# Performance work log

Measured on AMD Instinct MI355X. Metric: run time of the kernel, lower is better.

## Reference

```python
import jax, jax.numpy as jnp
import numpy as np

D_MODEL = 1024
B, S = 4, 2048


def setup_inputs() -> dict:
    key = jax.random.key(0)
    kx, km, kq, kk, kv, ko = jax.random.split(key, 6)
    x = jax.random.normal(kx, (B, S, D_MODEL), dtype=jnp.float32)
    mask = jax.random.randint(km, (B, S, S), 0, 2).astype(jnp.bool_)
    # flax Dense default kernel init: lecun_normal-ish; plain scaled normal is fine for a reference
    init_scale = 1.0 / np.sqrt(D_MODEL)
    Wq = jax.random.normal(kq, (D_MODEL, D_MODEL), dtype=jnp.float32) * init_scale
    Wk = jax.random.normal(kk, (D_MODEL, D_MODEL), dtype=jnp.float32) * init_scale
    Wv = jax.random.normal(kv, (D_MODEL, D_MODEL), dtype=jnp.float32) * init_scale
    Wo = jax.random.normal(ko, (D_MODEL, D_MODEL), dtype=jnp.float32) * init_scale
    return {"x": x, "mask": mask, "Wq": Wq, "Wk": Wk, "Wv": Wv, "Wo": Wo}


def reference(x, mask, Wq, Wk, Wv, Wo):
    # QKV projections (use_bias=False)
    q = jnp.einsum('bsd,de->bse', x, Wq)
    k = jnp.einsum('bsd,de->bse', x, Wk)
    v = jnp.einsum('bsd,de->bse', x, Wv)
    scale = jnp.sqrt(jnp.asarray(q.shape[-1], x.dtype)).astype(x.dtype)
    # [B, S, S] attention scores
    attn_scores = jnp.einsum('bqd,bkd->bqk', q, k) / scale
    attn_scores = jnp.where(mask, attn_scores, jnp.asarray(-1e10, x.dtype))
    attn_weights = jax.nn.softmax(attn_scores, axis=-1)
    attn_output = jnp.einsum('bqk,bkd->bqd', attn_weights, v)
    return jnp.einsum('bsd,de->bse', attn_output, Wo)
```

## Files before the change

kernel.cpp:

```cpp
#include <hip/hip_runtime.h>


#define DM 1024
#define SQ 2048
#define NB 4
typedef unsigned short U16;
typedef short bhalf8 __attribute__((ext_vector_type(8)));
typedef float f32x4 __attribute__((ext_vector_type(4)));

__device__ inline U16 f2bf(float f) {
  unsigned int u = __float_as_uint(f);
  u += 0x7FFFu + ((u >> 16) & 1u);
  return (U16)(u >> 16);
}
__device__ inline float2 bfp2(unsigned int u) {
  float2 r;
  r.x = __uint_as_float(u << 16);
  r.y = __uint_as_float(u & 0xffff0000u);
  return r;
}
__device__ inline unsigned int packbf(float a, float b) {
  return (unsigned int)f2bf(a) | ((unsigned int)f2bf(b) << 16);
}

__global__ __launch_bounds__(256) void conv_f32_bf16(
    const float* __restrict__ src, U16* __restrict__ dst) {
  int i = (blockIdx.x * 256 + threadIdx.x) * 8;
  float4 a = *(const float4*)(src + i);
  float4 b = *(const float4*)(src + i + 4);
  uint4 w;
  w.x = packbf(a.x, a.y); w.y = packbf(a.z, a.w);
  w.z = packbf(b.x, b.y); w.w = packbf(b.z, b.w);
  *(uint4*)(dst + i) = w;
}

__device__ inline void ldcvt16(const float* p, U16* d) {
#pragma unroll
  for (int i = 0; i < 4; ++i) {
    float4 f = *(const float4*)(p + i * 4);
    d[i * 4 + 0] = f2bf(f.x); d[i * 4 + 1] = f2bf(f.y);
    d[i * 4 + 2] = f2bf(f.z); d[i * 4 + 3] = f2bf(f.w);
  }
}
__device__ inline void ldcvt16(const U16* p, U16* d) {
  uint4 a = *(const uint4*)p;
  uint4 b = *(const uint4*)(p + 8);
  *(uint4*)d = a;
  *(uint4*)(d + 8) = b;
}
template <typename TIN>
__global__ __launch_bounds__(256) void transp_to_bf16(
    const TIN* __restrict__ src, U16* __restrict__ dst, int R, int C) {
  __shared__ U16 tile[64][72];
  const int z = blockIdx.z;
  src += (size_t)z * R * C;
  dst += (size_t)z * R * C;
  const int r0 = blockIdx.y * 64, c0 = blockIdx.x * 64;
  const int t = threadIdx.x;
  const int tr = t >> 2, tc = (t & 3) * 16;
  ldcvt16(src + (size_t)(r0 + tr) * C + c0 + tc, &tile[tr][tc]);
  __syncthreads();
  U16 vals[16];
#pragma unroll
  for (int m = 0; m < 16; ++m) vals[m] = tile[tc + m][tr];
  U16* op = dst + (size_t)(c0 + tr) * R + r0 + tc;
  *(uint4*)op = *(uint4*)&vals[0];
  *(uint4*)(op + 8) = *(uint4*)&vals[8];
}

template <int EP>
__global__ __launch_bounds__(256) void gemm_mfma(
    const U16* __restrict__ A, const U16* __restrict__ B, void* __restrict__ Cv,
    int M, int N, int K, long long sA, long long sB, long long sC,
    const int* __restrict__ mask, const float* __restrict__ rowsum, float scale) {
  __shared__ U16 As[128 * 72];
  __shared__ U16 Bs[128 * 72];
  const int t = threadIdx.x;
  const int lane = t & 63, wave = t >> 6;
  const int wm = wave >> 1, wn = wave & 1;
  const int q = lane >> 4, ln = lane & 15;
  const int z = blockIdx.z;
  const int m0 = blockIdx.y * 128, n0 = blockIdx.x * 128;
  A += (size_t)z * sA;
  B += (size_t)z * sB;

  f32x4 acc[4][4] = {};

  const int srow = t >> 3;
  const int scol = (t & 7) * 8;

  for (int k0 = 0; k0 < K; k0 += 64) {
    const U16* ga = A + (size_t)(m0 + srow) * K + k0 + scol;
    const U16* gb = B + (size_t)(n0 + srow) * K + k0 + scol;
#pragma unroll
    for (int it = 0; it < 4; ++it) {
      uint4 va = *(const uint4*)(ga + (size_t)it * 32 * K);
      uint4 vb = *(const uint4*)(gb + (size_t)it * 32 * K);
      *(uint4*)&As[(it * 32 + srow) * 72 + scol] = va;
      *(uint4*)&Bs[(it * 32 + srow) * 72 + scol] = vb;
    }
    __syncthreads();
#pragma unroll
    for (int kk = 0; kk < 64; kk += 32) {
      bhalf8 af[4], bg[4];
#pragma unroll
      for (int i = 0; i < 4; ++i) {
        af[i] = *(const bhalf8*)&As[(wm * 64 + i * 16 + ln) * 72 + kk + q * 8];
        bg[i] = *(const bhalf8*)&Bs[(wn * 64 + i * 16 + ln) * 72 + kk + q * 8];
      }
#pragma unroll
      for (int i = 0; i < 4; ++i)
#pragma unroll
        for (int j = 0; j < 4; ++j)
          acc[i][j] = __builtin_amdgcn_mfma_f32_16x16x32_bf16(af[i], bg[j], acc[i][j], 0, 0, 0);
    }
    __syncthreads();
  }

#pragma unroll
  for (int i = 0; i < 4; ++i) {
#pragma unroll
    for (int r = 0; r < 4; ++r) {
      const int rr = m0 + wm * 64 + i * 16 + q * 4 + r;
      float linv = 0.f;
      if constexpr (EP == 2) linv = 1.0f / rowsum[(size_t)z * M + rr];
#pragma unroll
      for (int j = 0; j < 4; ++j) {
        const int c = n0 + wn * 64 + j * 16 + ln;
        float v = acc[i][j][r];
        if constexpr (EP == 0) {
          ((U16*)Cv)[(size_t)z * sC + (size_t)rr * N + c] = f2bf(v);
        } else if constexpr (EP == 1) {
          int mk = mask[((size_t)z * M + rr) * N + c];
          float p = mk ? __expf(v * scale) : 0.f;
          ((U16*)Cv)[(size_t)z * sC + (size_t)rr * N + c] = f2bf(p);
        } else if constexpr (EP == 2) {
          ((U16*)Cv)[(size_t)z * sC + (size_t)rr * N + c] = f2bf(v * linv);
        } else {
          ((float*)Cv)[(size_t)z * sC + (size_t)rr * N + c] = v;
        }
      }
    }
  }
}

__global__ __launch_bounds__(256) void rowsum_k(
    const U16* __restrict__ P, float* __restrict__ rs) {
  const int t = threadIdx.x;
  const int w = t >> 6, lane = t & 63;
  const int row = blockIdx.x * 4 + w;
  const U16* p = P + (size_t)row * SQ;
  float s = 0.f;
#pragma unroll
  for (int it = 0; it < 4; ++it) {
    uint4 v = *(const uint4*)(p + it * 512 + lane * 8);
    float2 a = bfp2(v.x), b = bfp2(v.y), c = bfp2(v.z), d = bfp2(v.w);
    s += a.x + a.y + b.x + b.y + c.x + c.y + d.x + d.y;
  }
#pragma unroll
  for (int off = 32; off > 0; off >>= 1) s += __shfl_xor(s, off, 64);
  if (lane == 0) rs[row] = s + 1e-30f;
}

__device__ inline float4 load4(const float* p) { return *(const float4*)p; }
__device__ inline float4 load4(const U16* p) {
  uint2 w = *(const uint2*)p;
  float2 f0 = bfp2(w.x), f1 = bfp2(w.y);
  return make_float4(f0.x, f0.y, f1.x, f1.y);
}
__device__ inline void store4(float* p, float a, float b, float c, float d) {
  *(float4*)p = make_float4(a, b, c, d);
}
__device__ inline void store4(U16* p, float a, float b, float c, float d) {
  uint2 w;
  w.x = packbf(a, b);
  w.y = packbf(c, d);
  *(uint2*)p = w;
}
template <typename TA, typename TB, typename TC>
__global__ __launch_bounds__(256) void gemm_t(
    const TA* __restrict__ A, const TB* __restrict__ B,
    TC* __restrict__ C, int M, int N, int K) {
  __shared__ float As[16][64];
  __shared__ float Bs[16][64];
  const int t = threadIdx.x;
  const int tx = t & 15, ty = t >> 4;
  const int m0 = blockIdx.y * 64;
  const int n0 = blockIdx.x * 64;
  const int arow = t >> 2, akq = (t & 3) * 4;
  const int brow = t >> 4, bcg = (t & 15) * 4;
  float acc[4][4] = {};
  for (int k0 = 0; k0 < K; k0 += 16) {
    {
      float4 f = load4(A + (size_t)(m0 + arow) * K + k0 + akq);
      As[akq + 0][arow] = f.x; As[akq + 1][arow] = f.y;
      As[akq + 2][arow] = f.z; As[akq + 3][arow] = f.w;
    }
    {
      float4 f = load4(B + (size_t)(k0 + brow) * N + n0 + bcg);
      *(float4*)&Bs[brow][bcg] = f;
    }
    __syncthreads();
#pragma unroll
    for (int kk = 0; kk < 16; ++kk) {
      float4 a = *(const float4*)&As[kk][ty * 4];
      float4 b = *(const float4*)&Bs[kk][tx * 4];
      float av[4] = {a.x, a.y, a.z, a.w};
      float bv[4] = {b.x, b.y, b.z, b.w};
#pragma unroll
      for (int i = 0; i < 4; ++i)
#pragma unroll
        for (int j = 0; j < 4; ++j) acc[i][j] += av[i] * bv[j];
    }
    __syncthreads();
  }
#pragma unroll
  for (int i = 0; i < 4; ++i)
    store4(&C[(size_t)(m0 + ty * 4 + i) * N + n0 + tx * 4],
           acc[i][0], acc[i][1], acc[i][2], acc[i][3]);
}
__global__ __launch_bounds__(256) void flash_wave(
    const U16* __restrict__ Q, const U16* __restrict__ Kd,
    const U16* __restrict__ V, const int* __restrict__ mask,
    U16* __restrict__ O) {
  __shared__ float q_s[4][DM];
  const int t = threadIdx.x;
  const int w = t >> 6;
  const int lane = t & 63;
  const int row = blockIdx.x * 4 + w;
  const int b = row >> 11;
  const size_t bo = (size_t)b * SQ * DM;
  const size_t mrow0 = (size_t)row * SQ;
  {
    const U16* qp = Q + (size_t)row * DM + lane * 16;
    uint4 w0 = *(const uint4*)qp;
    uint4 w1 = *(const uint4*)(qp + 8);
    float* dst = &q_s[w][lane * 16];
    float2 f;
    f = bfp2(w0.x); dst[0] = f.x;  dst[1] = f.y;
    f = bfp2(w0.y); dst[2] = f.x;  dst[3] = f.y;
    f = bfp2(w0.z); dst[4] = f.x;  dst[5] = f.y;
    f = bfp2(w0.w); dst[6] = f.x;  dst[7] = f.y;
    f = bfp2(w1.x); dst[8] = f.x;  dst[9] = f.y;
    f = bfp2(w1.y); dst[10] = f.x; dst[11] = f.y;
    f = bfp2(w1.z); dst[12] = f.x; dst[13] = f.y;
    f = bfp2(w1.w); dst[14] = f.x; dst[15] = f.y;
  }
  __syncthreads();
  float m = -3.0e38f, l = 0.f;
  float o[16] = {};
  const int dbase = lane * 16;
  const float* qrow = q_s[w];
  for (int j0 = 0; j0 < SQ; j0 += 64) {
    float s;
    {
      const U16* kp = Kd + bo + (size_t)(j0 + lane) * DM;
      float acc = 0.f;
      for (int d = 0; d < DM; d += 8) {
        uint4 kw = *(const uint4*)(kp + d);
        float2 a0 = bfp2(kw.x), a1 = bfp2(kw.y), a2 = bfp2(kw.z), a3 = bfp2(kw.w);
        acc += qrow[d] * a0.x + qrow[d + 1] * a0.y + qrow[d + 2] * a1.x +
               qrow[d + 3] * a1.y + qrow[d + 4] * a2.x + qrow[d + 5] * a2.y +
               qrow[d + 6] * a3.x + qrow[d + 7] * a3.y;
      }
      s = acc * 0.03125f;
      if (mask[mrow0 + j0 + lane] == 0) s = -1e10f;
    }
    float ms = s;
#pragma unroll
    for (int off = 32; off > 0; off >>= 1) ms = fmaxf(ms, __shfl_xor(ms, off, 64));
    float mn = fmaxf(m, ms);
    float alpha = __expf(m - mn);
    float p = __expf(s - mn);
    float ps = p;
#pragma unroll
    for (int off = 32; off > 0; off >>= 1) ps += __shfl_xor(ps, off, 64);
    l = l * alpha + ps;
    m = mn;
#pragma unroll
    for (int k = 0; k < 16; ++k) o[k] *= alpha;
    const U16* vp = V + bo + (size_t)j0 * DM + dbase;
    for (int j = 0; j < 64; ++j) {
      float pj = __shfl(p, j, 64);
      uint4 v0 = *(const uint4*)(vp + (size_t)j * DM);
      uint4 v1 = *(const uint4*)(vp + (size_t)j * DM + 8);
      float2 f0 = bfp2(v0.x), f1 = bfp2(v0.y), f2 = bfp2(v0.z), f3 = bfp2(v0.w);
      float2 g0 = bfp2(v1.x), g1 = bfp2(v1.y), g2 = bfp2(v1.z), g3 = bfp2(v1.w);
      o[0] += pj * f0.x;  o[1] += pj * f0.y;  o[2] += pj * f1.x;  o[3] += pj * f1.y;
      o[4] += pj * f2.x;  o[5] += pj * f2.y;  o[6] += pj * f3.x;  o[7] += pj * f3.y;
      o[8] += pj * g0.x;  o[9] += pj * g0.y;  o[10] += pj * g1.x; o[11] += pj * g1.y;
      o[12] += pj * g2.x; o[13] += pj * g2.y; o[14] += pj * g3.x; o[15] += pj * g3.y;
    }
  }
  float linv = (l > 0.f) ? (1.0f / l) : 0.f;
  U16* op = O + (size_t)row * DM + dbase;
  uint4 r0, r1;
  r0.x = packbf(o[0] * linv, o[1] * linv);
  r0.y = packbf(o[2] * linv, o[3] * linv);
  r0.z = packbf(o[4] * linv, o[5] * linv);
  r0.w = packbf(o[6] * linv, o[7] * linv);
  r1.x = packbf(o[8] * linv, o[9] * linv);
  r1.y = packbf(o[10] * linv, o[11] * linv);
  r1.z = packbf(o[12] * linv, o[13] * linv);
  r1.w = packbf(o[14] * linv, o[15] * linv);
  *(uint4*)op = r0;
  *(uint4*)(op + 8) = r1;
}

extern "C" void kernel_launch(void* const* d_in, const int* in_sizes, int n_in,
                              void* d_out, int out_size, void* d_ws, size_t ws_size,
                              hipStream_t stream) {
  const float* x  = (const float*)d_in[0];
  const int* mask = (const int*)d_in[1];
  const float* Wq = (const float*)d_in[2];
  const float* Wk = (const float*)d_in[3];
  const float* Wv = (const float*)d_in[4];
  const float* Wo = (const float*)d_in[5];
  float* out = (float*)d_out;

  const size_t MB = 1u << 20;
  const size_t E = (size_t)NB * SQ * DM;
  const size_t WE = (size_t)DM * DM;

  if (ws_size >= 121 * MB) {
    char* ws = (char*)d_ws;
    U16* WT   = (U16*)ws;
    U16* x16  = (U16*)(ws + 8 * MB);
    U16* Q16  = (U16*)(ws + 24 * MB);
    U16* K16  = (U16*)(ws + 40 * MB);
    U16* V16  = (U16*)(ws + 56 * MB);
    U16* VT16 = (U16*)(ws + 72 * MB);
    U16* P16  = (U16*)(ws + 88 * MB);
    float* rs = (float*)(ws + 120 * MB);
    U16* O16  = Q16;

    conv_f32_bf16<<<dim3(E / (256 * 8)), 256, 0, stream>>>(x, x16);
    dim3 tw(16, 16, 1);
    transp_to_bf16<float><<<tw, 256, 0, stream>>>(Wq, WT + 0 * WE, DM, DM);
    transp_to_bf16<float><<<tw, 256, 0, stream>>>(Wk, WT + 1 * WE, DM, DM);
    transp_to_bf16<float><<<tw, 256, 0, stream>>>(Wv, WT + 2 * WE, DM, DM);
    transp_to_bf16<float><<<tw, 256, 0, stream>>>(Wo, WT + 3 * WE, DM, DM);

    dim3 gqkv(DM / 128, (NB * SQ) / 128, 1);
    gemm_mfma<0><<<gqkv, 256, 0, stream>>>(x16, WT + 0 * WE, Q16, NB * SQ, DM, DM,
                                           0, 0, 0, nullptr, nullptr, 0.f);
    gemm_mfma<0><<<gqkv, 256, 0, stream>>>(x16, WT + 1 * WE, K16, NB * SQ, DM, DM,
                                           0, 0, 0, nullptr, nullptr, 0.f);
    gemm_mfma<0><<<gqkv, 256, 0, stream>>>(x16, WT + 2 * WE, V16, NB * SQ, DM, DM,
                                           0, 0, 0, nullptr, nullptr, 0.f);

    transp_to_bf16<U16><<<dim3(DM / 64, SQ / 64, NB), 256, 0, stream>>>(V16, VT16, SQ, DM);

    gemm_mfma<1><<<dim3(SQ / 128, SQ / 128, NB), 256, 0, stream>>>(
        Q16, K16, P16, SQ, SQ, DM,
        (long long)SQ * DM, (long long)SQ * DM, (long long)SQ * SQ,
        mask, nullptr, 0.03125f);

    rowsum_k<<<dim3((NB * SQ) / 4), 256, 0, stream>>>(P16, rs);

    gemm_mfma<2><<<dim3(DM / 128, SQ / 128, NB), 256, 0, stream>>>(
        P16, VT16, O16, SQ, DM, SQ,
        (long long)SQ * SQ, (long long)DM * SQ, (long long)SQ * DM,
        nullptr, rs, 0.f);

    gemm_mfma<3><<<gqkv, 256, 0, stream>>>(O16, WT + 3 * WE, out, NB * SQ, DM, DM,
                                           0, 0, 0, nullptr, nullptr, 0.f);
  } else {
    U16* Kw = (U16*)d_ws;
    U16* Vw = Kw + E;
    U16* Qw = Vw + E;
    U16* Ow = Qw;
    dim3 blk(256);
    dim3 gg(DM / 64, (NB * SQ) / 64);
    gemm_t<float, float, U16><<<gg, blk, 0, stream>>>(x, Wk, Kw, NB * SQ, DM, DM);
    gemm_t<float, float, U16><<<gg, blk, 0, stream>>>(x, Wv, Vw, NB * SQ, DM, DM);
    gemm_t<float, float, U16><<<gg, blk, 0, stream>>>(x, Wq, Qw, NB * SQ, DM, DM);
    flash_wave<<<dim3((NB * SQ) / 4), blk, 0, stream>>>(Qw, Kw, Vw, mask, Ow);
    gemm_t<U16, float, float><<<gg, blk, 0, stream>>>(Ow, Wo, out, NB * SQ, DM, DM);
  }
}
```

Baseline: 375.6 us.

## Load GEMM tiles directly to LDS and batch QKV projections in one launch

The MFMA GEMM now stages A/B tiles with global_load_lds (direct global-to-LDS DMA), using a K-step of 32 and an unpadded 32-wide LDS layout instead of register round-trips with 64-wide padded tiles. The three Q/K/V projection GEMMs are merged into a single launch using blockIdx.z with weight and output strides. This removes VGPR staging and per-launch overhead, but halves work per sync and the unpadded layout may introduce LDS bank conflicts on fragment reads. It also relies on Q16/K16/V16 being laid out at stride E in the workspace, which holds given the 16MB spacing.

Measured after the change: 399.5 us. +6.4%, slower.

```diff
diff --git a/kernel.cpp b/kernel.cpp
--- a/kernel.cpp
+++ b/kernel.cpp
@@ -21,6 +21,12 @@
 }
 __device__ inline unsigned int packbf(float a, float b) {
   return (unsigned int)f2bf(a) | ((unsigned int)f2bf(b) << 16);
+}
+
+__device__ inline void gload16(const U16* g, U16* l) {
+  __builtin_amdgcn_global_load_lds(
+      (const __attribute__((address_space(1))) unsigned int*)g,
+      (__attribute__((address_space(3))) unsigned int*)l, 16, 0, 0);
 }
 
 __global__ __launch_bounds__(256) void conv_f32_bf16(
@@ -73,8 +79,8 @@
     const U16* __restrict__ A, const U16* __restrict__ B, void* __restrict__ Cv,
     int M, int N, int K, long long sA, long long sB, long long sC,
     const int* __restrict__ mask, const float* __restrict__ rowsum, float scale) {
-  __shared__ U16 As[128 * 72];
-  __shared__ U16 Bs[128 * 72];
+  __shared__ U16 As[128 * 32];
+  __shared__ U16 Bs[128 * 32];
   const int t = threadIdx.x;
   const int lane = t & 63, wave = t >> 6;
   const int wm = wave >> 1, wn = wave & 1;
@@ -86,34 +92,35 @@
 
   f32x4 acc[4][4] = {};
 
-  const int srow = t >> 3;
-  const int scol = (t & 7) * 8;
-
-  for (int k0 = 0; k0 < K; k0 += 64) {
-    const U16* ga = A + (size_t)(m0 + srow) * K + k0 + scol;
-    const U16* gb = B + (size_t)(n0 + srow) * K + k0 + scol;
-#pragma unroll
-    for (int it = 0; it < 4; ++it) {
-      uint4 va = *(const uint4*)(ga + (size_t)it * 32 * K);
-      uint4 vb = *(const uint4*)(gb + (size_t)it * 32 * K);
-      *(uint4*)&As[(it * 32 + srow) * 72 + scol] = va;
-      *(uint4*)&Bs[(it * 32 + srow) * 72 + scol] = vb;
-    }
+  const int rsub = lane >> 2;
+  const int csub = (lane & 3) * 8;
+  const U16* ga0 = A + (size_t)(m0 + wave * 32 + rsub) * K + csub;
+  const U16* ga1 = ga0 + (size_t)16 * K;
+  const U16* gb0 = B + (size_t)(n0 + wave * 32 + rsub) * K + csub;
+  const U16* gb1 = gb0 + (size_t)16 * K;
+  U16* la0 = As + wave * 1024;
+  U16* la1 = la0 + 512;
+  U16* lb0 = Bs + wave * 1024;
+  U16* lb1 = lb0 + 512;
+
+  for (int k0 = 0; k0 < K; k0 += 32) {
+    gload16(ga0, la0);
+    gload16(ga1, la1);
+    gload16(gb0, lb0);
+    gload16(gb1, lb1);
+    ga0 += 32; ga1 += 32; gb0 += 32; gb1 += 32;
     __syncthreads();
-#pragma unroll
-    for (int kk = 0; kk < 64; kk += 32) {
-      bhalf8 af[4], bg[4];
-#pragma unroll
-      for (int i = 0; i < 4; ++i) {
-        af[i] = *(const bhalf8*)&As[(wm * 64 + i * 16 + ln) * 72 + kk + q * 8];
-        bg[i] = *(const bhalf8*)&Bs[(wn * 64 + i * 16 + ln) * 72 + kk + q * 8];
-      }
-#pragma unroll
-      for (int i = 0; i < 4; ++i)
-#pragma unroll
-        for (int j = 0; j < 4; ++j)
-          acc[i][j] = __builtin_amdgcn_mfma_f32_16x16x32_bf16(af[i], bg[j], acc[i][j], 0, 0, 0);
-    }
+    bhalf8 af[4], bg[4];
+#pragma unroll
+    for (int i = 0; i < 4; ++i) {
+      af[i] = *(const bhalf8*)&As[(wm * 64 + i * 16 + ln) * 32 + q * 8];
+      bg[i] = *(const bhalf8*)&Bs[(wn * 64 + i * 16 + ln) * 32 + q * 8];
+    }
+#pragma unroll
+    for (int i = 0; i < 4; ++i)
+#pragma unroll
+      for (int j = 0; j < 4; ++j)
+        acc[i][j] = __builtin_amdgcn_mfma_f32_16x16x32_bf16(af[i], bg[j], acc[i][j], 0, 0, 0);
     __syncthreads();
   }
 
@@ -341,13 +348,9 @@
     transp_to_bf16<float><<<tw, 256, 0, stream>>>(Wv, WT + 2 * WE, DM, DM);
     transp_to_bf16<float><<<tw, 256, 0, stream>>>(Wo, WT + 3 * WE, DM, DM);
 
-    dim3 gqkv(DM / 128, (NB * SQ) / 128, 1);
-    gemm_mfma<0><<<gqkv, 256, 0, stream>>>(x16, WT + 0 * WE, Q16, NB * SQ, DM, DM,
-                                           0, 0, 0, nullptr, nullptr, 0.f);
-    gemm_mfma<0><<<gqkv, 256, 0, stream>>>(x16, WT + 1 * WE, K16, NB * SQ, DM, DM,
-                                           0, 0, 0, nullptr, nullptr, 0.f);
-    gemm_mfma<0><<<gqkv, 256, 0, stream>>>(x16, WT + 2 * WE, V16, NB * SQ, DM, DM,
-                                           0, 0, 0, nullptr, nullptr, 0.f);
+    gemm_mfma<0><<<dim3(DM / 128, (NB * SQ) / 128, 3), 256, 0, stream>>>(
+        x16, WT, Q16, NB * SQ, DM, DM,
+        0, (long long)WE, (long long)E, nullptr, nullptr, 0.f);
 
     transp_to_bf16<U16><<<dim3(DM / 64, SQ / 64, NB), 256, 0, stream>>>(V16, VT16, SQ, DM);
 
@@ -363,8 +366,9 @@
         (long long)SQ * SQ, (long long)DM * SQ, (long long)SQ * DM,
         nullptr, rs, 0.f);
 
-    gemm_mfma<3><<<gqkv, 256, 0, stream>>>(O16, WT + 3 * WE, out, NB * SQ, DM, DM,
-                                           0, 0, 0, nullptr, nullptr, 0.f);
+    gemm_mfma<3><<<dim3(DM / 128, (NB * SQ) / 128, 1), 256, 0, stream>>>(
+        O16, WT + 3 * WE, out, NB * SQ, DM, DM,
+        0, 0, 0, nullptr, nullptr, 0.f);
   } else {
     U16* Kw = (U16*)d_ws;
     U16* Vw = Kw + E;
```
